# Performance work log

Measured on AMD Instinct MI355X. Metric: run time of the kernel, lower is better.

Reference implementation:

```python
import jax, jax.numpy as jnp
import numpy as np
import math

B, L, DIM, H = 2, 2048, 512, 8


def setup_inputs() -> dict:
    key = jax.random.key(0)
    ks = jax.random.split(key, 8)
    s = 0.02
    return {
        "x": jax.random.normal(ks[0], (B, L, DIM), dtype=jnp.float32),
        "Wq": jax.random.normal(ks[1], (DIM, DIM), dtype=jnp.float32) * s,
        "Wk": jax.random.normal(ks[2], (DIM, DIM), dtype=jnp.float32) * s,
        "Wv": jax.random.normal(ks[3], (DIM, DIM), dtype=jnp.float32) * s,
        "Wb": jax.random.normal(ks[4], (H, DIM), dtype=jnp.float32) * s,   # content_bias weight
        "mixing": jax.random.normal(ks[5], (H, DIM), dtype=jnp.float32) * 0.2,  # UNIFORM init, std=0.2
        "Wd": jax.random.normal(ks[6], (DIM, DIM), dtype=jnp.float32) * s,
        "bd": jax.random.normal(ks[7], (DIM,), dtype=jnp.float32) * s,
    }


def reference(x, Wq, Wk, Wv, Wb, mixing, Wd, bd):
    b, l, d = x.shape
    h = mixing.shape[0]
    dh = d // h
    q = x @ Wq.T                      # [B,L,D]
    k = x @ Wk.T                      # [B,S,D]
    v = (x @ Wv.T).reshape(b, l, h, dh).transpose(0, 2, 1, 3)  # [B,H,S,dh]
    # scores[b,h,l,s] = sum_d q[b,l,d] * mixing[h,d] * k[b,s,d]
    scores = jnp.einsum("bld,hd,bsd->bhls", q, mixing, k)
    # content bias: [B,S,H] -> broadcast over query positions as [B,H,1,S]
    cb = jnp.einsum("bsd,hd->bhs", x, Wb)
    scale = math.sqrt(d / h)  # attention_head_size = dim / num_heads
    scores = (scores + cb[:, :, None, :]) / scale
    probs = jax.nn.softmax(scores, axis=-1)   # dropout disabled (eval)
    ctx = jnp.einsum("bhls,bhsd->bhld", probs, v)  # [B,H,L,dh]
    ctx = ctx.transpose(0, 2, 1, 3).reshape(b, l, d)
    return ctx @ Wd.T + bd
```

## Files before the change

### kernel.cpp

```cpp
#include <hip/hip_runtime.h>

#define B_ 2
#define L_ 2048
#define D_ 512
#define H_ 8
#define S_ 2048

typedef __attribute__((ext_vector_type(8))) short short8;
typedef __attribute__((ext_vector_type(8))) unsigned short ushort8;
typedef __attribute__((ext_vector_type(4))) unsigned short ushort4v;
typedef __attribute__((ext_vector_type(4))) float f32x4;
typedef __attribute__((ext_vector_type(16))) float f32x16;
typedef __attribute__((ext_vector_type(4))) float float4v;
typedef __attribute__((ext_vector_type(8))) _Float16 half8;

__device__ __forceinline__ unsigned short f2bf(float f) {
    unsigned u = __float_as_uint(f);
    u += 0x7FFF + ((u >> 16) & 1);
    return (unsigned short)(u >> 16);
}
__device__ __forceinline__ float bf2f(unsigned short s) {
    return __uint_as_float(((unsigned)s) << 16);
}
__device__ __forceinline__ unsigned char f2fp8(float f) {
    return (unsigned char)(__builtin_amdgcn_cvt_pk_fp8_f32(f, f, 0, false) & 0xff);
}
__device__ __forceinline__ long pack8fp8(const float* v) {
    int lo = __builtin_amdgcn_cvt_pk_fp8_f32(v[0], v[1], 0, false);
    lo = __builtin_amdgcn_cvt_pk_fp8_f32(v[2], v[3], lo, true);
    int hi = __builtin_amdgcn_cvt_pk_fp8_f32(v[4], v[5], 0, false);
    hi = __builtin_amdgcn_cvt_pk_fp8_f32(v[6], v[7], hi, true);
    union { int i[2]; long l; } u;
    u.i[0] = lo; u.i[1] = hi;
    return u.l;
}
__device__ __forceinline__ int swap23(int x) {
    return (x & ~12) | ((x & 4) << 1) | ((x & 8) >> 1);
}
__device__ __forceinline__ void async16(void* lds, const void* g) {
    __builtin_amdgcn_global_load_lds(
        (const __attribute__((address_space(1))) void*)(g),
        (__attribute__((address_space(3))) void*)(lds), 16, 0, 0);
}

__global__ __launch_bounds__(256) void cvt_cb(const float* __restrict__ x,
                                              const float* __restrict__ w0, const float* __restrict__ w1,
                                              const float* __restrict__ w2, const float* __restrict__ w3,
                                              const float* __restrict__ Wb,
                                              unsigned short* __restrict__ xb,
                                              unsigned short* __restrict__ d0, unsigned short* __restrict__ d1,
                                              unsigned short* __restrict__ d2, unsigned short* __restrict__ d3,
                                              float* __restrict__ cbf) {
    if (blockIdx.x < 3072) {
        int i = blockIdx.x * 256 + threadIdx.x;
        const float* s;
        unsigned short* d;
        int idx;
        if (i < 524288) { s = x; d = xb; idx = i; }
        else {
            int off = i - 524288;
            int wsel = off >> 16; idx = off & 65535;
            s = (wsel == 0) ? w0 : (wsel == 1) ? w1 : (wsel == 2) ? w2 : w3;
            d = (wsel == 0) ? d0 : (wsel == 1) ? d1 : (wsel == 2) ? d2 : d3;
        }
        float4v v = *(const float4v*)(s + (size_t)idx * 4);
        ushort4v o;
        o[0] = f2bf(v[0]); o[1] = f2bf(v[1]); o[2] = f2bf(v[2]); o[3] = f2bf(v[3]);
        *(ushort4v*)(d + (size_t)idx * 4) = o;
    } else {
        const int tid = threadIdx.x, w = tid >> 6, lane = tid & 63;
        const int row = (blockIdx.x - 3072) * 4 + w;
        const int h = lane >> 3, seg = lane & 7;
        const float* xp = x + (size_t)row * 512 + seg * 64;
        const float* wp = Wb + (size_t)h * 512 + seg * 64;
        float acc = 0.f;
        #pragma unroll
        for (int j = 0; j < 16; ++j) {
            float4v xv = *(const float4v*)(xp + j * 4);
            float4v wv = *(const float4v*)(wp + j * 4);
            acc += xv[0] * wv[0] + xv[1] * wv[1] + xv[2] * wv[2] + xv[3] * wv[3];
        }
        acc += __shfl_xor(acc, 1);
        acc += __shfl_xor(acc, 2);
        acc += __shfl_xor(acc, 4);
        if (seg == 0) {
            int b = row >> 11, s = row & 2047;
            int T = s >> 5, off = s & 31;
            int r2 = off & 3, k = off >> 2;
            int u = (k & 1) + ((k >> 2) << 1), hi2 = (k >> 1) & 1;
            int R = 4 * u + r2;
            cbf[((size_t)((b * 8 + h) * 64 + T)) * 32 + hi2 * 16 + R] = acc * 0.125f * 1.44269504f;
        }
    }
}

__device__ __forceinline__ void gemm128_core(const unsigned short* __restrict__ Ap,
                                             const unsigned short* __restrict__ Bp,
                                             short* sA, short* sB, int tid, f32x4 c[4][4]) {
    const int w = tid >> 6, lane = tid & 63, quad = lane >> 4, l15 = lane & 15;
    const int wm = (w >> 1) * 64, wn = (w & 1) * 64;
    for (int kc = 0; kc < 8; ++kc) {
        __syncthreads();
        #pragma unroll
        for (int j = 0; j < 4; ++j) {
            int i = tid + j * 256;
            int row = i >> 3, seg = i & 7;
            *(ushort8*)&sA[row * 72 + seg * 8] = *(const ushort8*)(Ap + (size_t)row * 512 + kc * 64 + seg * 8);
            *(ushort8*)&sB[row * 72 + seg * 8] = *(const ushort8*)(Bp + (size_t)row * 512 + kc * 64 + seg * 8);
        }
        __syncthreads();
        #pragma unroll
        for (int ks = 0; ks < 2; ++ks) {
            short8 a[4], b[4];
            #pragma unroll
            for (int ii = 0; ii < 4; ++ii)
                a[ii] = *(const short8*)&sA[(wm + ii * 16 + l15) * 72 + ks * 32 + quad * 8];
            #pragma unroll
            for (int jj = 0; jj < 4; ++jj)
                b[jj] = *(const short8*)&sB[(wn + jj * 16 + l15) * 72 + ks * 32 + quad * 8];
            #pragma unroll
            for (int ii = 0; ii < 4; ++ii)
                #pragma unroll
                for (int jj = 0; jj < 4; ++jj)
                    c[ii][jj] = __builtin_amdgcn_mfma_f32_16x16x32_bf16(a[ii], b[jj], c[ii][jj], 0, 0, 0);
        }
    }
}

__global__ __launch_bounds__(256) void gemm_qkv(const unsigned short* __restrict__ xb,
                                                const unsigned short* __restrict__ Wqb,
                                                const unsigned short* __restrict__ Wkb,
                                                const unsigned short* __restrict__ Wvb,
                                                unsigned short* __restrict__ qb,
                                                unsigned char* __restrict__ kpack8,
                                                unsigned short* __restrict__ vfrag) {
    __shared__ short sA[128 * 72];
    __shared__ short sB[128 * 72];
    const int m0 = blockIdx.x * 128, n0 = blockIdx.y * 128, z = blockIdx.z;
    const unsigned short* Bsel = (z == 0) ? Wqb : ((z == 1) ? Wkb : Wvb);
    f32x4 c[4][4];
    #pragma unroll
    for (int ii = 0; ii < 4; ++ii)
        #pragma unroll
        for (int jj = 0; jj < 4; ++jj) { f32x4 zv = {0.f, 0.f, 0.f, 0.f}; c[ii][jj] = zv; }
    gemm128_core(xb + (size_t)m0 * 512, Bsel + (size_t)n0 * 512, sA, sB, threadIdx.x, c);
    const int tid = threadIdx.x, w = tid >> 6, lane = tid & 63, quad = lane >> 4, l15 = lane & 15;
    const int wm = (w >> 1) * 64, wn = (w & 1) * 64;
    #pragma unroll
    for (int ii = 0; ii < 4; ++ii) {
        const int mb = m0 + wm + ii * 16 + quad * 4;
        const int bb = mb >> 11;
        if (z == 0) {
            #pragma unroll
            for (int jj = 0; jj < 4; ++jj) {
                int ncol = n0 + wn + jj * 16 + l15;
                #pragma unroll
                for (int r = 0; r < 4; ++r)
                    qb[(size_t)(mb + r) * 512 + ncol] = f2bf(c[ii][jj][r]);
            }
        } else if (z == 1) {
            #pragma unroll
            for (int jj = 0; jj < 4; ++jj) {
                int d = n0 + wn + jj * 16 + l15;
                int pair = d >> 5, fh = (d >> 4) & 1, hid = (d >> 3) & 1, jq = d & 7;
                #pragma unroll
                for (int r = 0; r < 4; ++r) {
                    int s = (mb + r) & 2047;
                    int t = s >> 5, rr = swap23(s & 31);
                    kpack8[(((size_t)(bb * 64 + t) * 16 + pair) << 10)
                           + (hid * 32 + rr) * 16 + fh * 8 + jq] = f2fp8(c[ii][jj][r] * 32.f);
                }
            }
        } else {
            const int hh = (n0 + wn) >> 6;
            const int s = mb & 2047;
            #pragma unroll
            for (int jj = 0; jj < 4; ++jj) {
                int dh = jj * 16 + l15;
                ushort4v o;
                o[0] = f2bf(c[ii][jj][0]); o[1] = f2bf(c[ii][jj][1]);
                o[2] = f2bf(c[ii][jj][2]); o[3] = f2bf(c[ii][jj][3]);
                size_t blk = ((size_t)(bb * H_ + hh) * 64 + (s >> 5)) * 4
                           + ((dh >> 5) * 2 + ((s >> 4) & 1));
                *(ushort4v*)(vfrag + blk * 512 + (dh & 31) * 8 + ((s >> 3) & 1) * 256 + (s & 7)) = o;
            }
        }
    }
}

__global__ __launch_bounds__(256) void gemm_out(const _Float16* __restrict__ Opart,
                                                const float* __restrict__ lpart,
                                                const unsigned short* __restrict__ Wdb,
                                                const float* __restrict__ bd,
                                                float* __restrict__ out) {
    __shared__ short sA[128 * 72];
    __shared__ short sB[128 * 72];
    const int m0 = blockIdx.x * 128, n0 = blockIdx.y * 128;
    const int tid = threadIdx.x, w = tid >> 6, lane = tid & 63, quad = lane >> 4, l15 = lane & 15;
    const int wm = (w >> 1) * 64, wn = (w & 1) * 64;
    f32x4 c[4][4];
    #pragma unroll
    for (int ii = 0; ii < 4; ++ii)
        #pragma unroll
        for (int jj = 0; jj < 4; ++jj) { f32x4 zv = {0.f, 0.f, 0.f, 0.f}; c[ii][jj] = zv; }
    for (int kc = 0; kc < 8; ++kc) {
        __syncthreads();
        #pragma unroll
        for (int j = 0; j < 4; ++j) {
            int i = tid + j * 256;
            int row = i >> 3, seg = i & 7;
            int gq = m0 + row;
            int b = gq >> 11, ql = gq & 2047, qq = ql & 127;
            int base = ((ql >> 7) << 5) | (kc << 2) | (b << 1);
            const _Float16* o0 = Opart + ((size_t)base << 13) + qq * 64 + seg * 8;
            float l = lpart[(size_t)base * 128 + qq] + lpart[(size_t)(base + 1) * 128 + qq];
            float inv = __builtin_amdgcn_rcpf(l);
            half8 v0 = *(const half8*)o0;
            half8 v1 = *(const half8*)(o0 + 8192);
            ushort8 ov;
            #pragma unroll
            for (int e = 0; e < 8; ++e)
                ov[e] = f2bf(((float)v0[e] + (float)v1[e]) * inv);
            *(ushort8*)&sA[row * 72 + seg * 8] = ov;
            *(ushort8*)&sB[row * 72 + seg * 8] =
                *(const ushort8*)(Wdb + (size_t)(n0 + row) * 512 + kc * 64 + seg * 8);
        }
        __syncthreads();
        #pragma unroll
        for (int ks = 0; ks < 2; ++ks) {
            short8 a[4], b2[4];
            #pragma unroll
            for (int ii = 0; ii < 4; ++ii)
                a[ii] = *(const short8*)&sA[(wm + ii * 16 + l15) * 72 + ks * 32 + quad * 8];
            #pragma unroll
            for (int jj = 0; jj < 4; ++jj)
                b2[jj] = *(const short8*)&sB[(wn + jj * 16 + l15) * 72 + ks * 32 + quad * 8];
            #pragma unroll
            for (int ii = 0; ii < 4; ++ii)
                #pragma unroll
                for (int jj = 0; jj < 4; ++jj)
                    c[ii][jj] = __builtin_amdgcn_mfma_f32_16x16x32_bf16(a[ii], b2[jj], c[ii][jj], 0, 0, 0);
        }
    }
    #pragma unroll
    for (int ii = 0; ii < 4; ++ii) {
        const int mb = m0 + wm + ii * 16 + quad * 4;
        #pragma unroll
        for (int jj = 0; jj < 4; ++jj) {
            int ncol = n0 + wn + jj * 16 + l15;
            float bias = bd[ncol];
            #pragma unroll
            for (int r = 0; r < 4; ++r)
                out[(size_t)(mb + r) * 512 + ncol] = c[ii][jj][r] + bias;
        }
    }
}

__global__ __launch_bounds__(256, 2) void flash_attn(const unsigned short* __restrict__ qb,
                                                     const unsigned char* __restrict__ kpack8,
                                                     const unsigned short* __restrict__ vfrag,
                                                     const float* __restrict__ cbf_all,
                                                     const float* __restrict__ mixing,
                                                     _Float16* __restrict__ Opart,
                                                     float* __restrict__ lpart) {
    __shared__ char sK[3][16384];
    const int bid = blockIdx.x;
    const int half = bid & 1, b = (bid >> 1) & 1, h = (bid >> 2) & 7, qt = bid >> 5;
    const int tid = threadIdx.x, w = tid >> 6, lane = tid & 63;
    const int l31 = lane & 31, hi = lane >> 5;
    const int q0 = qt * 128 + w * 32;
    const unsigned short* vfb = vfrag + ((size_t)(b * H_ + h) * 64 + half * 32) * 2048;
    const float* cbfb = cbf_all + ((size_t)((b * 8 + h) * 64 + half * 32)) * 32 + hi * 16;
    const float* mixh = mixing + h * D_;
    const float SC = 1.44269504f / 4096.0f;

    long qq[32];
    {
        const unsigned short* qrow = qb + ((size_t)(b * L_) + q0 + l31) * D_ + hi * 8;
        #pragma unroll
        for (int i = 0; i < 32; ++i) {
            ushort8 qv = *(const ushort8*)(qrow + i * 16);
            float4v ma = *(const float4v*)(mixh + i * 16 + hi * 8);
            float4v mb = *(const float4v*)(mixh + i * 16 + hi * 8 + 4);
            float v[8];
            v[0] = bf2f(qv[0]) * ma[0] * 16.f;
            v[1] = bf2f(qv[1]) * ma[1] * 16.f;
            v[2] = bf2f(qv[2]) * ma[2] * 16.f;
            v[3] = bf2f(qv[3]) * ma[3] * 16.f;
            v[4] = bf2f(qv[4]) * mb[0] * 16.f;
            v[5] = bf2f(qv[5]) * mb[1] * 16.f;
            v[6] = bf2f(qv[6]) * mb[2] * 16.f;
            v[7] = bf2f(qv[7]) * mb[3] * 16.f;
            qq[i] = pack8fp8(v);
        }
    }
    asm volatile("s_waitcnt vmcnt(0)" ::: "memory");

    f32x16 acco0, acco1;
    #pragma unroll
    for (int i = 0; i < 16; ++i) { acco0[i] = 0.f; acco1[i] = 0.f; }
    float lsum = 0.f;
    f32x16 aA0, aB0, aA1, aB1;
    short8 av00, av01, av10, av11;
    float4v cbf0, cbf1, cbf2, cbf3;

    auto stageK2 = [&](int t, int bi) {
        const char* src = (const char*)kpack8 + (((size_t)(b * 64 + half * 32 + t)) << 14);
        char* dst = &sK[bi][0];
        #pragma unroll
        for (int ii = 0; ii < 4; ++ii)
            async16(dst + w * 1024 + ii * 4096, src + w * 1024 + ii * 4096 + (size_t)lane * 16);
    };
    auto ldV = [&](int t) {
        const unsigned short* vp = vfb + (size_t)t * 2048 + lane * 8;
        av00 = *(const short8*)(vp);
        av01 = *(const short8*)(vp + 512);
        av10 = *(const short8*)(vp + 1024);
        av11 = *(const short8*)(vp + 1536);
        asm volatile("" ::: "memory");
    };
    auto ldCB = [&](int t) {
        const float* cp = cbfb + t * 32;
        cbf0 = *(const float4v*)(cp);
        cbf1 = *(const float4v*)(cp + 4);
        cbf2 = *(const float4v*)(cp + 8);
        cbf3 = *(const float4v*)(cp + 12);
        asm volatile("" ::: "memory");
    };
    auto cbfv = [&](int R) -> float {
        return (R < 4) ? cbf0[R & 3] : (R < 8) ? cbf1[R & 3] : (R < 12) ? cbf2[R & 3] : cbf3[R & 3];
    };
    auto pack_pv = [&](const float* pex) {
        union { unsigned int u[4]; short8 s8; } P0, P1;
        #pragma unroll
        for (int j = 0; j < 4; ++j) {
            P0.u[j] = __builtin_amdgcn_perm(__float_as_uint(pex[2 * j + 1]) + 0x8000u,
                                            __float_as_uint(pex[2 * j]) + 0x8000u, 0x07060302u);
            P1.u[j] = __builtin_amdgcn_perm(__float_as_uint(pex[8 + 2 * j + 1]) + 0x8000u,
                                            __float_as_uint(pex[8 + 2 * j]) + 0x8000u, 0x07060302u);
        }
        acco0 = __builtin_amdgcn_mfma_f32_32x32x16_bf16(av00, P0.s8, acco0, 0, 0, 0);
        acco0 = __builtin_amdgcn_mfma_f32_32x32x16_bf16(av01, P1.s8, acco0, 0, 0, 0);
        acco1 = __builtin_amdgcn_mfma_f32_32x32x16_bf16(av10, P0.s8, acco1, 0, 0, 0);
        acco1 = __builtin_amdgcn_mfma_f32_32x32x16_bf16(av11, P1.s8, acco1, 0, 0, 0);
    };
    auto tile_fused = [&](const char* buf, int T, f32x16& CA, f32x16& CB,
                          const f32x16& PA, const f32x16& PB) {
        __builtin_amdgcn_s_setprio(1);
        float pex[16];
        float lsA = 0.f, lsB = 0.f;
        #pragma unroll
        for (int fp = 0; fp < 16; ++fp) {
            const long* ap = (const long*)&buf[fp * 1024 + lane * 16];
            long a0 = ap[0], a1 = ap[1];
            CA = __builtin_amdgcn_mfma_f32_32x32x16_fp8_fp8(a0, qq[2 * fp], CA, 0, 0, 0);
            CB = __builtin_amdgcn_mfma_f32_32x32x16_fp8_fp8(a1, qq[2 * fp + 1], CB, 0, 0, 0);
            if (fp < 8) {
                float x0 = fmaf(PA[2 * fp] + PB[2 * fp], SC, cbfv(2 * fp));
                float x1 = fmaf(PA[2 * fp + 1] + PB[2 * fp + 1], SC, cbfv(2 * fp + 1));
                float e0, e1;
                asm("v_exp_f32 %0, %1" : "=v"(e0) : "v"(x0));
                asm("v_exp_f32 %0, %1" : "=v"(e1) : "v"(x1));
                pex[2 * fp] = e0; pex[2 * fp + 1] = e1;
                lsA += e0; lsB += e1;
            }
            if (fp == 8) { lsum += lsA + lsB; pack_pv(pex); }
            if (fp == 9)  ldV(T);
            if (fp == 10) ldCB(T);
        }
        __builtin_amdgcn_s_setprio(0);
    };
    auto tile_plain = [&](const char* buf, int T, f32x16& CA, f32x16& CB) {
        __builtin_amdgcn_s_setprio(1);
        #pragma unroll
        for (int fp = 0; fp < 16; ++fp) {
            const long* ap = (const long*)&buf[fp * 1024 + lane * 16];
            long a0 = ap[0], a1 = ap[1];
            CA = __builtin_amdgcn_mfma_f32_32x32x16_fp8_fp8(a0, qq[2 * fp], CA, 0, 0, 0);
            CB = __builtin_amdgcn_mfma_f32_32x32x16_fp8_fp8(a1, qq[2 * fp + 1], CB, 0, 0, 0);
            if (fp == 9)  ldV(T);
            if (fp == 10) ldCB(T);
        }
        __builtin_amdgcn_s_setprio(0);
    };
    auto sm_pv = [&](const f32x16& PA, const f32x16& PB) {
        float pex[16];
        float lsA = 0.f, lsB = 0.f;
        #pragma unroll
        for (int R = 0; R < 16; R += 2) {
            float x0 = fmaf(PA[R] + PB[R], SC, cbfv(R));
            float x1 = fmaf(PA[R + 1] + PB[R + 1], SC, cbfv(R + 1));
            float e0, e1;
            asm("v_exp_f32 %0, %1" : "=v"(e0) : "v"(x0));
            asm("v_exp_f32 %0, %1" : "=v"(e1) : "v"(x1));
            pex[R] = e0; pex[R + 1] = e1;
            lsA += e0; lsB += e1;
        }
        lsum += lsA + lsB;
        pack_pv(pex);
    };
    auto zero16 = [](f32x16& v) {
        #pragma unroll
        for (int i = 0; i < 16; ++i) v[i] = 0.f;
    };

    stageK2(0, 0); stageK2(1, 1);

    zero16(aA0); zero16(aB0);
    asm volatile("s_waitcnt vmcnt(4)" ::: "memory");
    __builtin_amdgcn_s_barrier();
    tile_plain(&sK[0][0], 0, aA0, aB0);
    stageK2(2, 2);

    int cur = 1;
    for (int t = 1; t <= 30; t += 2) {
        zero16(aA1); zero16(aB1);
        asm volatile("s_waitcnt vmcnt(4)" ::: "memory");
        __builtin_amdgcn_s_barrier();
        tile_fused(&sK[cur][0], t, aA1, aB1, aA0, aB0);
        if (t + 2 <= 31) stageK2(t + 2, (cur + 2 >= 3) ? cur - 1 : cur + 2);
        cur = (cur == 2) ? 0 : cur + 1;

        zero16(aA0); zero16(aB0);
        asm volatile("s_waitcnt vmcnt(4)" ::: "memory");
        __builtin_amdgcn_s_barrier();
        tile_fused(&sK[cur][0], t + 1, aA0, aB0, aA1, aB1);
        if (t + 3 <= 31) stageK2(t + 3, (cur + 2 >= 3) ? cur - 1 : cur + 2);
        cur = (cur == 2) ? 0 : cur + 1;
    }

    {
        zero16(aA1); zero16(aB1);
        asm volatile("s_waitcnt vmcnt(0)" ::: "memory");
        __builtin_amdgcn_s_barrier();
        tile_fused(&sK[cur][0], 31, aA1, aB1, aA0, aB0);
        asm volatile("s_waitcnt vmcnt(0)" ::: "memory");
        sm_pv(aA1, aB1);
    }

    lsum += __shfl_xor(lsum, 32);
    if (hi == 0) lpart[(size_t)bid * 128 + w * 32 + l31] = lsum;
    __syncthreads();
    {
        _Float16* sO = (_Float16*)&sK[0][0];
        const int q = w * 32 + l31;
        #pragma unroll
        for (int R = 0; R < 16; ++R) {
            int dh = (R & 3) + 8 * (R >> 2) + 4 * hi;
            sO[q * 72 + dh]      = (_Float16)acco0[R];
            sO[q * 72 + 32 + dh] = (_Float16)acco1[R];
        }
        const int qd = tid >> 1, hf = tid & 1;
        _Float16* dst = Opart + ((size_t)bid << 13) + qd * 64 + hf * 32;
        const _Float16* srcp = sO + qd * 72 + hf * 32;
        #pragma unroll
        for (int k = 0; k < 4; ++k)
            *(half8*)(dst + k * 8) = *(const half8*)(srcp + k * 8);
    }
}

extern "C" void kernel_launch(void* const* d_in, const int* in_sizes, int n_in,
                              void* d_out, int out_size, void* d_ws, size_t ws_size,
                              hipStream_t stream) {
    (void)in_sizes; (void)n_in; (void)out_size; (void)ws_size;
    const float* x      = (const float*)d_in[0];
    const float* Wq     = (const float*)d_in[1];
    const float* Wk     = (const float*)d_in[2];
    const float* Wv     = (const float*)d_in[3];
    const float* Wb     = (const float*)d_in[4];
    const float* mixing = (const float*)d_in[5];
    const float* Wd     = (const float*)d_in[6];
    const float* bd     = (const float*)d_in[7];
    float* out = (float*)d_out;

    char* ws = (char*)d_ws;
    const size_t MiB = 1048576;
    unsigned short* xb     = (unsigned short*)(ws);
    unsigned short* qb     = (unsigned short*)(ws + 4 * MiB);
    unsigned char*  kpack8 = (unsigned char*)(ws + 8 * MiB);
    unsigned short* vfrag  = (unsigned short*)(ws + 10 * MiB);
    unsigned short* Wqb    = (unsigned short*)(ws + 18 * MiB);
    unsigned short* Wkb    = (unsigned short*)(ws + 18 * MiB + 512 * 1024);
    unsigned short* Wvb    = (unsigned short*)(ws + 19 * MiB);
    unsigned short* Wdb    = (unsigned short*)(ws + 19 * MiB + 512 * 1024);
    float* cbuf            = (float*)(ws + 20 * MiB);
    float* lpart           = (float*)(ws + 20 * MiB + 256 * 1024);
    _Float16* Opart        = (_Float16*)(ws + 21 * MiB);

    cvt_cb<<<4096, 256, 0, stream>>>(x, Wq, Wk, Wv, Wd, Wb, xb, Wqb, Wkb, Wvb, Wdb, cbuf);
    gemm_qkv<<<dim3(32, 4, 3), 256, 0, stream>>>(xb, Wqb, Wkb, Wvb, qb, kpack8, vfrag);
    flash_attn<<<512, 256, 0, stream>>>(qb, kpack8, vfrag, cbuf, mixing, Opart, lpart);
    gemm_out<<<dim3(32, 4), 256, 0, stream>>>(Opart, lpart, Wdb, bd, out);
}
```

Measured before the change: 197.0 us.

## Double-buffer QKV GEMM with async swizzled LDS loads; vectorize output stores

Replaces the shared gemm128_core call in the QKV projection kernel with an inline loop. The loop double-buffers 128-wide K chunks in LDS through async 16-byte global-to-LDS copies, using an XOR swizzle to avoid bank conflicts. The intent is to overlap global loads with MFMA work. In the attention epilogue, per-element fp16 LDS stores become half4 vector stores, and a __syncthreads before writing into the reused sK buffer is removed, which risks a race if other waves still read sK.

```diff
diff --git a/kernel.cpp b/kernel.cpp
--- a/kernel.cpp
+++ b/kernel.cpp
@@ -13,6 +13,7 @@
 typedef __attribute__((ext_vector_type(16))) float f32x16;
 typedef __attribute__((ext_vector_type(4))) float float4v;
 typedef __attribute__((ext_vector_type(8))) _Float16 half8;
+typedef __attribute__((ext_vector_type(4))) _Float16 half4;
 
 __device__ __forceinline__ unsigned short f2bf(float f) {
     unsigned u = __float_as_uint(f);
@@ -134,18 +135,59 @@
                                                 unsigned short* __restrict__ qb,
                                                 unsigned char* __restrict__ kpack8,
                                                 unsigned short* __restrict__ vfrag) {
-    __shared__ short sA[128 * 72];
-    __shared__ short sB[128 * 72];
+    __shared__ char sAB[2][32768];
     const int m0 = blockIdx.x * 128, n0 = blockIdx.y * 128, z = blockIdx.z;
     const unsigned short* Bsel = (z == 0) ? Wqb : ((z == 1) ? Wkb : Wvb);
+    const int tid = threadIdx.x, w = tid >> 6, lane = tid & 63, quad = lane >> 4, l15 = lane & 15;
+    const int wm = (w >> 1) * 64, wn = (w & 1) * 64;
+    const char* Ab = (const char*)(xb + (size_t)m0 * 512);
+    const char* Bb = (const char*)(Bsel + (size_t)n0 * 512);
+    const int srow = tid >> 3;
+    const int csw = (tid & 7) ^ (srow & 7);
+    const size_t srcOff = (size_t)srow * 1024 + (size_t)csw * 16;
+    auto stage = [&](int kc, int bi) {
+        char* ba = &sAB[bi][0];
+        #pragma unroll
+        for (int j = 0; j < 4; ++j)
+            async16(ba + j * 4096 + w * 1024, Ab + (size_t)j * 32768 + kc * 128 + srcOff);
+        #pragma unroll
+        for (int j = 0; j < 4; ++j)
+            async16(ba + 16384 + j * 4096 + w * 1024, Bb + (size_t)j * 32768 + kc * 128 + srcOff);
+    };
+
     f32x4 c[4][4];
     #pragma unroll
     for (int ii = 0; ii < 4; ++ii)
         #pragma unroll
         for (int jj = 0; jj < 4; ++jj) { f32x4 zv = {0.f, 0.f, 0.f, 0.f}; c[ii][jj] = zv; }
-    gemm128_core(xb + (size_t)m0 * 512, Bsel + (size_t)n0 * 512, sA, sB, threadIdx.x, c);
-    const int tid = threadIdx.x, w = tid >> 6, lane = tid & 63, quad = lane >> 4, l15 = lane & 15;
-    const int wm = (w >> 1) * 64, wn = (w & 1) * 64;
+
+    stage(0, 0);
+    for (int kc = 0; kc < 8; ++kc) {
+        __syncthreads();
+        if (kc < 7) stage(kc + 1, (kc + 1) & 1);
+        const char* tA = &sAB[kc & 1][0];
+        const char* tB = &sAB[kc & 1][16384];
+        #pragma unroll
+        for (int ks = 0; ks < 2; ++ks) {
+            short8 a[4], b[4];
+            #pragma unroll
+            for (int ii = 0; ii < 4; ++ii) {
+                int row = wm + ii * 16 + l15;
+                a[ii] = *(const short8*)(tA + row * 128 + (((ks * 4 + quad) ^ (l15 & 7)) * 16));
+            }
+            #pragma unroll
+            for (int jj = 0; jj < 4; ++jj) {
+                int row = wn + jj * 16 + l15;
+                b[jj] = *(const short8*)(tB + row * 128 + (((ks * 4 + quad) ^ (l15 & 7)) * 16));
+            }
+            #pragma unroll
+            for (int ii = 0; ii < 4; ++ii)
+                #pragma unroll
+                for (int jj = 0; jj < 4; ++jj)
+                    c[ii][jj] = __builtin_amdgcn_mfma_f32_16x16x32_bf16(a[ii], b[jj], c[ii][jj], 0, 0, 0);
+        }
+    }
+
     #pragma unroll
     for (int ii = 0; ii < 4; ++ii) {
         const int mb = m0 + wm + ii * 16 + quad * 4;
@@ -440,15 +482,18 @@
 
     lsum += __shfl_xor(lsum, 32);
     if (hi == 0) lpart[(size_t)bid * 128 + w * 32 + l31] = lsum;
-    __syncthreads();
     {
         _Float16* sO = (_Float16*)&sK[0][0];
         const int q = w * 32 + l31;
         #pragma unroll
-        for (int R = 0; R < 16; ++R) {
-            int dh = (R & 3) + 8 * (R >> 2) + 4 * hi;
-            sO[q * 72 + dh]      = (_Float16)acco0[R];
-            sO[q * 72 + 32 + dh] = (_Float16)acco1[R];
+        for (int u = 0; u < 4; ++u) {
+            half4 v0, v1;
+            v0[0] = (_Float16)acco0[4 * u];     v0[1] = (_Float16)acco0[4 * u + 1];
+            v0[2] = (_Float16)acco0[4 * u + 2]; v0[3] = (_Float16)acco0[4 * u + 3];
+            v1[0] = (_Float16)acco1[4 * u];     v1[1] = (_Float16)acco1[4 * u + 1];
+            v1[2] = (_Float16)acco1[4 * u + 2]; v1[3] = (_Float16)acco1[4 * u + 3];
+            *(half4*)&sO[q * 72 + u * 8 + 4 * hi]      = v0;
+            *(half4*)&sO[q * 72 + 32 + u * 8 + 4 * hi] = v1;
         }
         const int qd = tid >> 1, hf = tid & 1;
         _Float16* dst = Opart + ((size_t)bid << 13) + qd * 64 + hf * 32;
```

After: 193.6 us, median of 2. No clear change (-1.8%).
